# Kernel tuning notes

Measured on AMD Instinct MI355X. Metric: run time of the kernel, lower is better.

Reference implementation:

```python
import jax, jax.numpy as jnp
import numpy as np

SHIFTS = 1
WINDOW_SIZES = (4, 8, 16)
BN_EPS = 1e-5


def _calc_attn_path(x, ws, shifts):
    # x: (b, H, W, 2c) with channels laid out as (qv=2, c)
    b, H, W, c2 = x.shape
    c = c2 // 2
    if shifts > 0:
        x = jnp.roll(x, shift=(-ws // 2, -ws // 2), axis=(1, 2))
    h, w = H // ws, W // ws
    # 'b (h dh) (w dw) (qv c) -> qv (b h w) (dh dw c)'
    qv = x.reshape(b, h, ws, w, ws, 2, c).transpose(5, 0, 1, 3, 2, 4, 6)
    qv = qv.reshape(2, b * h * w, ws * ws * c)
    q, v = qv[0], qv[1]                       # (N, D), N = b*h*w windows, D = ws*ws*c
    atn = jax.nn.softmax(q @ q.T, axis=-1)    # (N, N) attention across windows (as in source)
    y = atn @ v                               # (N, D)
    # '(b h w) (dh dw c) -> b (h dh) (w dw) c'
    y = y.reshape(b, h, w, ws, ws, c).transpose(0, 1, 3, 2, 4, 5).reshape(b, H, W, c)
    if shifts > 0:
        y = jnp.roll(y, shift=(ws // 2, ws // 2), axis=(1, 2))
    return y, atn


def setup_inputs() -> dict:
    key = jax.random.key(0)
    ks = jax.random.split(key, 3)
    B, H, W, C = 4, 128, 128, 180
    inputs = jax.random.normal(ks[0], (B, H, W, C), jnp.float32)
    conv1_w = jax.random.normal(ks[1], (1, 1, C, 2 * C), jnp.float32) * 0.05
    conv1_b = jnp.zeros((2 * C,), jnp.float32)
    bn_scale = jnp.ones((2 * C,), jnp.float32)
    bn_bias = jnp.zeros((2 * C,), jnp.float32)
    conv2_w = jax.random.normal(ks[2], (1, 1, C, C), jnp.float32) * 0.05
    conv2_b = jnp.zeros((C,), jnp.float32)
    return {"inputs": inputs, "conv1_w": conv1_w, "conv1_b": conv1_b,
            "bn_scale": bn_scale, "bn_bias": bn_bias,
            "conv2_w": conv2_w, "conv2_b": conv2_b}


def reference(inputs, conv1_w, conv1_b, bn_scale, bn_bias, conv2_w, conv2_b):
    # 1x1 conv to 2*C channels (calc_attn=True)
    x = jnp.einsum('bhwc,cd->bhwd', inputs, conv1_w[0, 0]) + conv1_b
    # BatchNorm in training mode (batch statistics)
    mean = x.mean(axis=(0, 1, 2))
    var = x.var(axis=(0, 1, 2))
    x = (x - mean) * jax.lax.rsqrt(var + BN_EPS) * bn_scale + bn_bias
    xs = jnp.split(x, 3, axis=-1)             # three groups of 2*C/3 channels
    ys, attns = [], []
    for ws, xi in zip(WINDOW_SIZES, xs):
        y, a = _calc_attn_path(xi, ws, SHIFTS)
        ys.append(y)
        attns.append(a)
    y = jnp.concatenate(ys, axis=-1)          # back to C channels
    y = jnp.einsum('bhwc,cd->bhwd', y, conv2_w[0, 0]) + conv2_b
    return (y, *attns)
```

## Files before the change

kernel.cpp:

```cpp
#include <hip/hip_runtime.h>

typedef unsigned short u16;
typedef __bf16 bf16x8 __attribute__((ext_vector_type(8)));
typedef float f32x4 __attribute__((ext_vector_type(4)));
typedef u16 u16x4 __attribute__((ext_vector_type(4)));
typedef u16 u16x8 __attribute__((ext_vector_type(8)));

__device__ __forceinline__ u16 f2bf(float v) {
    unsigned u = __float_as_uint(v);
    unsigned r = (u + 0x7fffu + ((u >> 16) & 1u)) >> 16;
    return (u16)r;
}
__device__ __forceinline__ float bf2f(u16 u) { return __uint_as_float(((unsigned)u) << 16); }

__device__ __forceinline__ void async_cp16(const u16* g, u16* l) {
    __builtin_amdgcn_global_load_lds((const __attribute__((address_space(1))) unsigned int*)g,
                                     (__attribute__((address_space(3))) unsigned int*)l, 16, 0, 0);
}

__global__ __launch_bounds__(256) void gemm_f32(
    const u16* __restrict__ A, const u16* __restrict__ B,
    float* __restrict__ C, const float* __restrict__ bias,
    int K, int ldc, int n_store)
{
    __shared__ char smem[16384];
    u16* As = (u16*)smem;
    u16* Bs = (u16*)(smem + 8192);
    const int tid = threadIdx.x;
    const int lane = tid & 63;
    const int wave = tid >> 6;
    const int wm = wave >> 1, wn = wave & 1;
    const long m0 = (long)blockIdx.y * 128;
    const long n0 = (long)blockIdx.x * 128;

    f32x4 acc[4][4] = {};
    const int lrow = tid >> 2;
    const int lk = (tid & 3) << 3;
    const u16* Ag = A + (m0 + lrow) * (long)K + lk;
    const u16* Bg = B + (n0 + lrow) * (long)K + lk;
    u16* Asl = As + tid * 8;
    u16* Bsl = Bs + tid * 8;
    const long K64 = (long)64 * K;

    for (int k0 = 0; k0 < K; k0 += 32) {
        async_cp16(Ag + k0, Asl);
        async_cp16(Ag + k0 + K64, Asl + 2048);
        async_cp16(Bg + k0, Bsl);
        async_cp16(Bg + k0 + K64, Bsl + 2048);
        __syncthreads();
        bf16x8 af[4], bg[4];
        const int ro = (lane & 15) * 32 + ((lane >> 4) << 3);
#pragma unroll
        for (int i = 0; i < 4; i++) af[i] = *(const bf16x8*)(As + (wm * 64 + i * 16) * 32 + ro);
#pragma unroll
        for (int j = 0; j < 4; j++) bg[j] = *(const bf16x8*)(Bs + (wn * 64 + j * 16) * 32 + ro);
#pragma unroll
        for (int i = 0; i < 4; i++)
#pragma unroll
            for (int j = 0; j < 4; j++)
                acc[i][j] = __builtin_amdgcn_mfma_f32_16x16x32_bf16(af[i], bg[j], acc[i][j], 0, 0, 0);
        __syncthreads();
    }

    float bv[4];
#pragma unroll
    for (int j = 0; j < 4; j++) bv[j] = bias[n0 + wn * 64 + j * 16 + (lane & 15)];

    float* Cs = (float*)smem;
    for (int c = 0; c < 4; c++) {
        __syncthreads();
        if (wm == (c >> 1)) {
#pragma unroll
            for (int ii = 0; ii < 2; ii++) {
                const int i = (c & 1) * 2 + ii;
#pragma unroll
                for (int j = 0; j < 4; j++)
#pragma unroll
                    for (int r = 0; r < 4; r++) {
                        const int lr = ii * 16 + ((lane >> 4) << 2) + r;
                        Cs[lr * 128 + wn * 64 + j * 16 + (lane & 15)] = acc[i][j][r] + bv[j];
                    }
            }
        }
        __syncthreads();
        const int lr = tid >> 3;
        const int cg = (tid & 7) * 16;
        const long rowg = m0 + c * 32 + lr;
#pragma unroll
        for (int e = 0; e < 4; e++) {
            const int colg = cg + e * 4;
            if ((int)n0 + colg < n_store)
                *(f32x4*)(C + rowg * (long)ldc + n0 + colg) = *(const f32x4*)(Cs + lr * 128 + colg);
        }
    }
}

__global__ __launch_bounds__(256) void conv1_gemm(
    const float* __restrict__ A, const u16* __restrict__ B,
    u16* __restrict__ C, const float* __restrict__ bias)
{
    __shared__ char smem[16384];
    u16* As = (u16*)smem;
    u16* Bs = (u16*)(smem + 8192);
    const int tid = threadIdx.x;
    const int lane = tid & 63;
    const int wave = tid >> 6;
    const int wm = wave >> 1, wn = wave & 1;
    const long m0 = (long)blockIdx.y * 128;
    const long n0 = (long)blockIdx.x * 128;

    f32x4 acc[4][4] = {};
    const int lrow = tid >> 2;
    const int lk = (tid & 3) << 3;
    const float* Ar0 = A + (m0 + lrow) * 180L;
    const float* Ar1 = Ar0 + 64 * 180L;
    const u16* Bg = B + (n0 + lrow) * 192L + lk;
    u16* Asl = As + tid * 8;
    u16* Bsl = Bs + tid * 8;

#pragma unroll
    for (int k0 = 0; k0 < 192; k0 += 32) {
        const int gk = k0 + lk;
        u16x8 oa, ob;
        if (gk + 8 <= 180) {
            f32x4 a0 = *(const f32x4*)(Ar0 + gk), a1 = *(const f32x4*)(Ar0 + gk + 4);
            f32x4 b0 = *(const f32x4*)(Ar1 + gk), b1 = *(const f32x4*)(Ar1 + gk + 4);
#pragma unroll
            for (int c = 0; c < 4; c++) {
                oa[c] = f2bf(a0[c]); oa[4 + c] = f2bf(a1[c]);
                ob[c] = f2bf(b0[c]); ob[4 + c] = f2bf(b1[c]);
            }
        } else if (gk < 180) {
            f32x4 a0 = *(const f32x4*)(Ar0 + gk);
            f32x4 b0 = *(const f32x4*)(Ar1 + gk);
#pragma unroll
            for (int c = 0; c < 4; c++) {
                oa[c] = f2bf(a0[c]); oa[4 + c] = 0;
                ob[c] = f2bf(b0[c]); ob[4 + c] = 0;
            }
        } else {
#pragma unroll
            for (int c = 0; c < 8; c++) { oa[c] = 0; ob[c] = 0; }
        }
        *(u16x8*)Asl = oa;
        *(u16x8*)(Asl + 2048) = ob;
        async_cp16(Bg + k0, Bsl);
        async_cp16(Bg + k0 + 64 * 192, Bsl + 2048);
        __syncthreads();
        bf16x8 af[4], bg[4];
        const int ro = (lane & 15) * 32 + ((lane >> 4) << 3);
#pragma unroll
        for (int i = 0; i < 4; i++) af[i] = *(const bf16x8*)(As + (wm * 64 + i * 16) * 32 + ro);
#pragma unroll
        for (int j = 0; j < 4; j++) bg[j] = *(const bf16x8*)(Bs + (wn * 64 + j * 16) * 32 + ro);
#pragma unroll
        for (int i = 0; i < 4; i++)
#pragma unroll
            for (int j = 0; j < 4; j++)
                acc[i][j] = __builtin_amdgcn_mfma_f32_16x16x32_bf16(af[i], bg[j], acc[i][j], 0, 0, 0);
        __syncthreads();
    }

    float bv[4];
#pragma unroll
    for (int j = 0; j < 4; j++) bv[j] = bias[n0 + wn * 64 + j * 16 + (lane & 15)];

    u16* Cs = (u16*)smem;
    for (int c = 0; c < 2; c++) {
        __syncthreads();
        if (wm == c) {
#pragma unroll
            for (int i = 0; i < 4; i++)
#pragma unroll
                for (int j = 0; j < 4; j++)
#pragma unroll
                    for (int r = 0; r < 4; r++) {
                        const int lr = i * 16 + ((lane >> 4) << 2) + r;
                        Cs[lr * 128 + wn * 64 + j * 16 + (lane & 15)] = f2bf(acc[i][j][r] + bv[j]);
                    }
        }
        __syncthreads();
        const int lr = tid >> 2;
        const int cg = (tid & 3) * 32;
        const long rowg = m0 + c * 64 + lr;
#pragma unroll
        for (int e = 0; e < 4; e++) {
            const int colg = cg + e * 8;
            *(u16x8*)(C + rowg * 384L + n0 + colg) = *(const u16x8*)(Cs + lr * 128 + colg);
        }
    }
}

__global__ __launch_bounds__(256) void qq_all(
    const u16* __restrict__ q0, const u16* __restrict__ q1, const u16* __restrict__ q2,
    float* __restrict__ S0, float* __restrict__ pG1, float* __restrict__ pG2)
{
    __shared__ char smem[16384];
    u16* As = (u16*)smem;
    u16* Bs = (u16*)(smem + 8192);
    const int bid = blockIdx.x;
    int seg, local;
    if (bid < 528) { seg = 0; local = bid; }
    else if (bid < 816) { seg = 1; local = bid - 528; }
    else { seg = 2; local = bid - 816; }
    const int tX = seg == 0 ? 32 : (seg == 1 ? 8 : 2);
    const int TT = (tX * (tX + 1)) >> 1;
    const int K = seg == 0 ? 1024 : (seg == 1 ? 3840 : 15360);
    const int Ksplit = seg == 0 ? 1024 : (seg == 1 ? 480 : 256);
    const int N = seg == 0 ? 4096 : (seg == 1 ? 1024 : 256);
    const u16* A = seg == 0 ? q0 : (seg == 1 ? q1 : q2);
    float* outP = seg == 0 ? S0 : (seg == 1 ? pG1 : pG2);
    const int z = local / TT;
    int rem = local - z * TT;
    int by = 0, rowlen = tX;
    while (rem >= rowlen) { rem -= rowlen; by++; rowlen--; }
    const int bx = by + rem;

    const int tid = threadIdx.x;
    const int lane = tid & 63;
    const int wave = tid >> 6;
    const int wm = wave >> 1, wn = wave & 1;
    const long m0 = (long)by * 128;
    const long n0 = (long)bx * 128;
    const int kbeg = z * Ksplit;

    f32x4 acc[4][4] = {};
    const int lrow = tid >> 2;
    const int lk = (tid & 3) << 3;
    const u16* Ag = A + (m0 + lrow) * (long)K + lk;
    const u16* Bg = A + (n0 + lrow) * (long)K + lk;
    u16* Asl = As + tid * 8;
    u16* Bsl = Bs + tid * 8;
    const long K64 = (long)64 * K;

    for (int k0 = kbeg; k0 < kbeg + Ksplit; k0 += 32) {
        async_cp16(Ag + k0, Asl);
        async_cp16(Ag + k0 + K64, Asl + 2048);
        async_cp16(Bg + k0, Bsl);
        async_cp16(Bg + k0 + K64, Bsl + 2048);
        __syncthreads();
        bf16x8 af[4], bg[4];
        const int ro = (lane & 15) * 32 + ((lane >> 4) << 3);
#pragma unroll
        for (int i = 0; i < 4; i++) af[i] = *(const bf16x8*)(As + (wm * 64 + i * 16) * 32 + ro);
#pragma unroll
        for (int j = 0; j < 4; j++) bg[j] = *(const bf16x8*)(Bs + (wn * 64 + j * 16) * 32 + ro);
#pragma unroll
        for (int i = 0; i < 4; i++)
#pragma unroll
            for (int j = 0; j < 4; j++)
                acc[i][j] = __builtin_amdgcn_mfma_f32_16x16x32_bf16(af[i], bg[j], acc[i][j], 0, 0, 0);
        __syncthreads();
    }

    float* Pz = outP + (long)z * N * N;

    if (bx != by) {
        const int r0 = (int)n0 + wn * 64 + (lane & 15);
        const int c0 = (int)m0 + wm * 64 + ((lane >> 4) << 2);
#pragma unroll
        for (int j = 0; j < 4; j++) {
            float* rp = Pz + (long)(r0 + j * 16) * N + c0;
#pragma unroll
            for (int i = 0; i < 4; i++)
                *(f32x4*)(rp + i * 16) = acc[i][j];
        }
    }

    float* Cs = (float*)smem;
    for (int c = 0; c < 4; c++) {
        __syncthreads();
        if (wm == (c >> 1)) {
#pragma unroll
            for (int ii = 0; ii < 2; ii++) {
                const int i = (c & 1) * 2 + ii;
#pragma unroll
                for (int j = 0; j < 4; j++)
#pragma unroll
                    for (int r = 0; r < 4; r++) {
                        const int lr = ii * 16 + ((lane >> 4) << 2) + r;
                        Cs[lr * 128 + wn * 64 + j * 16 + (lane & 15)] = acc[i][j][r];
                    }
            }
        }
        __syncthreads();
        const int lr = tid >> 3;
        const int cg = (tid & 7) * 16;
        const long rowg = m0 + c * 32 + lr;
#pragma unroll
        for (int e = 0; e < 4; e++) {
            const int colg = cg + e * 4;
            *(f32x4*)(Pz + rowg * (long)N + n0 + colg) = *(const f32x4*)(Cs + lr * 128 + colg);
        }
    }
}

__global__ __launch_bounds__(256, 4) void pv_all(
    const u16* __restrict__ a0, const u16* __restrict__ a1, const u16* __restrict__ a2,
    const u16* __restrict__ vt0, const u16* __restrict__ vt1, const u16* __restrict__ vt2,
    u16* __restrict__ Ysp, float* __restrict__ pP0, float* __restrict__ pP1)
{
    __shared__ char smem[16384];
    u16* As = (u16*)smem;
    u16* Bs = (u16*)(smem + 8192);
    const int bid = blockIdx.x;
    int seg, local, z = 0;
    if (bid < 512) { seg = 0; z = bid >> 8; local = bid & 255; }
    else if (bid < 752) { seg = 1; local = bid - 512; }
    else { seg = 2; local = bid - 752; }
    const int tX = seg == 0 ? 8 : (seg == 1 ? 30 : 120);
    const int K = seg == 0 ? 4096 : (seg == 1 ? 1024 : 256);
    const int Ksplit = seg == 0 ? 2048 : K;
    const int D = seg == 0 ? 960 : (seg == 1 ? 3840 : 15360);
    const int l2ws = 2 + seg;
    const int l2wc = 5 - seg;
    const u16* A = seg == 0 ? a0 : (seg == 1 ? a1 : a2);
    const u16* B = seg == 0 ? vt0 : (seg == 1 ? vt1 : vt2);
    const int bx = local % tX;
    const int by = local / tX;

    const int tid = threadIdx.x;
    const int lane = tid & 63;
    const int wave = tid >> 6;
    const int wm = wave >> 1, wn = wave & 1;
    const long m0 = (long)by * 128;
    const long n0 = (long)bx * 128;
    const int kbeg = z * Ksplit;

    f32x4 acc[4][4] = {};
    const int lrow = tid >> 2;
    const int lk = (tid & 3) << 3;
    const u16* Ag = A + (m0 + lrow) * (long)K + lk;
    const u16* Bg = B + (n0 + lrow) * (long)K + lk;
    u16* Asl = As + tid * 8;
    u16* Bsl = Bs + tid * 8;
    const long K64 = (long)64 * K;

    for (int k0 = kbeg; k0 < kbeg + Ksplit; k0 += 32) {
        async_cp16(Ag + k0, Asl);
        async_cp16(Ag + k0 + K64, Asl + 2048);
        async_cp16(Bg + k0, Bsl);
        async_cp16(Bg + k0 + K64, Bsl + 2048);
        __syncthreads();
        bf16x8 af[4], bg[4];
        const int ro = (lane & 15) * 32 + ((lane >> 4) << 3);
#pragma unroll
        for (int i = 0; i < 4; i++) af[i] = *(const bf16x8*)(As + (wm * 64 + i * 16) * 32 + ro);
#pragma unroll
        for (int j = 0; j < 4; j++) bg[j] = *(const bf16x8*)(Bs + (wn * 64 + j * 16) * 32 + ro);
#pragma unroll
        for (int i = 0; i < 4; i++)
#pragma unroll
            for (int j = 0; j < 4; j++)
                acc[i][j] = __builtin_amdgcn_mfma_f32_16x16x32_bf16(af[i], bg[j], acc[i][j], 0, 0, 0);
        __syncthreads();
    }

    if (seg == 0) {
        float* Pz = (z == 0) ? pP0 : pP1;
        float* Cs = (float*)smem;
        for (int c = 0; c < 4; c++) {
            __syncthreads();
            if (wm == (c >> 1)) {
#pragma unroll
                for (int ii = 0; ii < 2; ii++) {
                    const int i = (c & 1) * 2 + ii;
#pragma unroll
                    for (int j = 0; j < 4; j++)
#pragma unroll
                        for (int r = 0; r < 4; r++) {
                            const int lr = ii * 16 + ((lane >> 4) << 2) + r;
                            Cs[lr * 128 + wn * 64 + j * 16 + (lane & 15)] = acc[i][j][r];
                        }
                }
            }
            __syncthreads();
            const int lr = tid >> 3;
            const int cg = (tid & 7) * 16;
            const long rowg = m0 + c * 32 + lr;
#pragma unroll
            for (int e = 0; e < 4; e++) {
                const int colg = cg + e * 4;
                *(f32x4*)(Pz + rowg * 1024L + n0 + colg) = *(const f32x4*)(Cs + lr * 128 + colg);
            }
        }
        return;
    }

    u16* Cs = (u16*)smem;
    const int wcm = (1 << l2wc) - 1;
    const int wsm = (1 << l2ws) - 1;
    const int sh = 1 << (l2ws - 1);
    for (int c = 0; c < 2; c++) {
        __syncthreads();
        if (wm == c) {
#pragma unroll
            for (int i = 0; i < 4; i++)
#pragma unroll
                for (int j = 0; j < 4; j++)
#pragma unroll
                    for (int r = 0; r < 4; r++) {
                        const int lr = i * 16 + ((lane >> 4) << 2) + r;
                        Cs[lr * 128 + wn * 64 + j * 16 + (lane & 15)] = f2bf(acc[i][j][r]);
                    }
        }
        __syncthreads();
        const int lr = tid >> 2;
        const int cgbase = (tid & 3) * 32;
        const int n = (int)m0 + c * 64 + lr;
        const int wi = n & wcm;
        const int hi = (n >> l2wc) & wcm;
        const int bb = n >> (2 * l2wc);
        const int rowb = (hi << l2ws) + sh;
        const int colb = (wi << l2ws) + sh;
        const long bbase = (long)bb * 128 * 128 * 192 + 60 * seg;
#pragma unroll
        for (int e = 0; e < 8; e++) {
            const int colg = cgbase + e * 4;
            const int d = (int)n0 + colg;
            if (d < D) {
                const int cc = d % 60;
                const int pp = d / 60;
                const int dh = pp >> l2ws;
                const int dw = pp & wsm;
                const int row = (rowb + dh) & 127;
                const int col = (colb + dw) & 127;
                *(u16x4*)(Ysp + bbase + ((long)row * 128 + col) * 192 + cc) =
                    *(const u16x4*)(Cs + lr * 128 + colg);
            }
        }
    }
}

__global__ __launch_bounds__(256) void reduce_scatter_g0(
    const float* __restrict__ pP0, const float* __restrict__ pP1, u16* __restrict__ Ysp)
{
    const int n = blockIdx.x;
    const int d = threadIdx.x * 4;
    if (d >= 960) return;
    const long i = (long)n * 1024 + d;
    f32x4 s = *(const f32x4*)(pP0 + i) + *(const f32x4*)(pP1 + i);
    const int cc = d % 60;
    const int pp = d / 60;
    const int dh = pp >> 2;
    const int dw = pp & 3;
    const int wi = n & 31;
    const int hi = (n >> 5) & 31;
    const int b = n >> 10;
    const int row = ((hi << 2) + dh + 2) & 127;
    const int col = ((wi << 2) + dw + 2) & 127;
    u16x4 o;
#pragma unroll
    for (int c = 0; c < 4; c++) o[c] = f2bf(s[c]);
    *(u16x4*)(Ysp + ((long)((b << 7) + row) * 128 + col) * 192 + cc) = o;
}

__global__ __launch_bounds__(256) void zero_pad(u16* __restrict__ Ysp)
{
    const long r = (long)blockIdx.x * 256 + threadIdx.x;
    u16* p = Ysp + r * 192 + 180;
    const u16x4 z = {0, 0, 0, 0};
    *(u16x4*)(p) = z;
    *(u16x4*)(p + 4) = z;
    *(u16x4*)(p + 8) = z;
}

__global__ __launch_bounds__(192) void prep_all(
    const float* __restrict__ W1, const float* __restrict__ W2,
    const float* __restrict__ b1, const float* __restrict__ b2,
    u16* __restrict__ W1t, u16* __restrict__ W2t,
    float* __restrict__ b1p, float* __restrict__ b2p, float* __restrict__ accum)
{
    const int bid = blockIdx.x;
    const int t = threadIdx.x;
    if (bid < 384) {
        W1t[bid * 192 + t] = (bid < 360 && t < 180) ? f2bf(W1[t * 360 + bid]) : (u16)0;
    } else if (bid < 640) {
        const int n = bid - 384;
        W2t[n * 192 + t] = (n < 180 && t < 180) ? f2bf(W2[t * 180 + n]) : (u16)0;
    } else {
#pragma unroll
        for (int j = 0; j < 4; j++) {
            const int i = t + 192 * j;
            if (i < 384) b1p[i] = (i < 360) ? b1[i] : 0.0f;
            else if (i < 640) { const int k = i - 384; b2p[k] = (k < 180) ? b2[k] : 0.0f; }
            if (i < 768) accum[i] = 0.0f;
        }
    }
}

__global__ __launch_bounds__(384) void bn_stats(const u16* __restrict__ x, float* __restrict__ accum)
{
    const int ch = threadIdx.x;
    const long base = (long)blockIdx.x * 256 * 384;
    float s = 0.0f, s2 = 0.0f;
    for (int r = 0; r < 256; r++) {
        const float v = bf2f(x[base + (long)r * 384 + ch]);
        s += v; s2 += v * v;
    }
    atomicAdd(&accum[ch], s);
    atomicAdd(&accum[384 + ch], s2);
}

__global__ __launch_bounds__(256) void gather_all(
    const u16* __restrict__ x, const float* __restrict__ accum,
    const float* __restrict__ bns, const float* __restrict__ bnb,
    u16* __restrict__ q0, u16* __restrict__ q1, u16* __restrict__ q2,
    u16* __restrict__ vt0, u16* __restrict__ vt1, u16* __restrict__ vt2)
{
    __shared__ u16 t[64][65];
    const int bid = blockIdx.x;
    int seg, local;
    if (bid < 1024) { seg = 0; local = bid; }
    else if (bid < 1984) { seg = 1; local = bid - 1024; }
    else { seg = 2; local = bid - 1984; }
    const int tX = seg == 0 ? 16 : (seg == 1 ? 60 : 240);
    const int N = seg == 0 ? 4096 : (seg == 1 ? 1024 : 256);
    const int D = seg == 0 ? 960 : (seg == 1 ? 3840 : 15360);
    const int Dp = seg == 0 ? 1024 : (seg == 1 ? 3840 : 15360);
    const int l2ws = 2 + seg;
    const int l2wc = 5 - seg;
    u16* q = seg == 0 ? q0 : (seg == 1 ? q1 : q2);
    u16* vt = seg == 0 ? vt0 : (seg == 1 ? vt1 : vt2);
    const int bx = local % tX;
    const int by = local / tX;

    const int d0 = bx * 64;
    const int n0 = by * 64;
    const int tc = threadIdx.x & 63;
    const int tr = threadIdx.x >> 6;

    const int d = d0 + tc;
    const int sh = 1 << (l2ws - 1);
    const int cc = d % 60;
    const int pp = d / 60;
    const int dh = pp >> l2ws;
    const int dw = pp & ((1 << l2ws) - 1);
    const int wcm = (1 << l2wc) - 1;
    const int ch = 120 * seg + cc;
    const float m_q = accum[ch] * (1.0f / 65536.0f);
    const float v_q = accum[384 + ch] * (1.0f / 65536.0f) - m_q * m_q;
    const float seq = bns[ch] * rsqrtf(v_q + 1e-5f);
    const float beq = bnb[ch] - m_q * seq;
    const float m_v = accum[ch + 60] * (1.0f / 65536.0f);
    const float v_v = accum[384 + ch + 60] * (1.0f / 65536.0f) - m_v * m_v;
    const float sev = bns[ch + 60] * rsqrtf(v_v + 1e-5f);
    const float bev = bnb[ch + 60] - m_v * sev;
    const bool valid = d < D;

#pragma unroll 4
    for (int i = 0; i < 16; i++) {
        const int n = n0 + i * 4 + tr;
        const int wi = n & wcm;
        const int hi = (n >> l2wc) & wcm;
        const int b = n >> (2 * l2wc);
        const int row = ((hi << l2ws) + dh + sh) & 127;
        const int col = ((wi << l2ws) + dw + sh) & 127;
        const long src = ((long)((b << 7) + row) * 128 + col) * 384 + ch;
        const float xq = bf2f(x[src]);
        const float xv = bf2f(x[src + 60]);
        q[(long)n * Dp + d] = valid ? f2bf(seq * xq + beq) : (u16)0;
        t[tc][i * 4 + tr] = f2bf(sev * xv + bev);
    }
    __syncthreads();
#pragma unroll 4
    for (int i = 0; i < 16; i++) {
        const int dd = i * 4 + tr;
        vt[(long)(d0 + dd) * N + n0 + tc] = t[dd][tc];
    }
}

template <int VPT>
__device__ __forceinline__ void softmax_body(
    const float* __restrict__ P, int nsplit, long MN, int rowi,
    float* __restrict__ S, u16* __restrict__ Sb)
{
    const int N = VPT * 256;
    const long base = (long)rowi * N;
    float v[VPT];
    float mx = -3.0e38f;
#pragma unroll
    for (int i = 0; i < VPT; i++) {
        const long idx = base + i * 256 + threadIdx.x;
        float val = P[idx];
        for (int z = 1; z < nsplit; z++) val += P[(long)z * MN + idx];
        v[i] = val; mx = fmaxf(mx, val);
    }
#pragma unroll
    for (int o = 32; o > 0; o >>= 1) mx = fmaxf(mx, __shfl_down(mx, o, 64));
    __shared__ float redm[4];
    if ((threadIdx.x & 63) == 0) redm[threadIdx.x >> 6] = mx;
    __syncthreads();
    mx = fmaxf(fmaxf(redm[0], redm[1]), fmaxf(redm[2], redm[3]));
    float s = 0.0f;
#pragma unroll
    for (int i = 0; i < VPT; i++) { v[i] = __expf(v[i] - mx); s += v[i]; }
#pragma unroll
    for (int o = 32; o > 0; o >>= 1) s += __shfl_down(s, o, 64);
    __shared__ float reds[4];
    if ((threadIdx.x & 63) == 0) reds[threadIdx.x >> 6] = s;
    __syncthreads();
    s = reds[0] + reds[1] + reds[2] + reds[3];
    const float inv = 1.0f / s;
#pragma unroll
    for (int i = 0; i < VPT; i++) {
        const float r = v[i] * inv;
        const long idx = base + i * 256 + threadIdx.x;
        S[idx] = r;
        Sb[idx] = f2bf(r);
    }
}

__global__ __launch_bounds__(256) void softmax_all(
    float* __restrict__ S0, const float* __restrict__ pG1, const float* __restrict__ pG2,
    float* __restrict__ out1, float* __restrict__ out2,
    u16* __restrict__ ab0, u16* __restrict__ ab1, u16* __restrict__ ab2)
{
    const int r = blockIdx.x;
    if (r < 4096)      softmax_body<16>(S0, 1, 16777216L, r, S0, ab0);
    else if (r < 5120) softmax_body<4>(pG1, 8, 1048576L, r - 4096, out1, ab1);
    else               softmax_body<1>(pG2, 60, 65536L, r - 5120, out2, ab2);
}

extern "C" void kernel_launch(void* const* d_in, const int* in_sizes, int n_in,
                              void* d_out, int out_size, void* d_ws, size_t ws_size,
                              hipStream_t stream)
{
    const float* in_x = (const float*)d_in[0];
    const float* w1  = (const float*)d_in[1];
    const float* b1  = (const float*)d_in[2];
    const float* bns = (const float*)d_in[3];
    const float* bnb = (const float*)d_in[4];
    const float* w2  = (const float*)d_in[5];
    const float* b2  = (const float*)d_in[6];
    float* out = (float*)d_out;

    char* w = (char*)d_ws;
    u16* atnb0 = (u16*)w;
    size_t off = 33554432;
    u16* x = (u16*)(w + off);
    float* pG1 = (float*)(w + off);
    float* pG2 = (float*)(w + off + 33554432);
    u16* Ysp = (u16*)(w + off);
    float* pP1 = (float*)(w + off + 25165824);
    off += 50331648;
    u16* W1t = (u16*)(w + off);  off += 147456;
    u16* W2t = (u16*)(w + off);  off += 98304;
    float* b1p = (float*)(w + off);   off += 4096;
    float* b2p = (float*)(w + off);   off += 4096;
    float* accum = (float*)(w + off); off += 4096;
    u16* q0 = (u16*)(w + off);  off += 8388608;
    u16* q1 = (u16*)(w + off);  off += 7864320;
    u16* q2 = (u16*)(w + off);  off += 7864320;
    u16* vt0 = (u16*)(w + off); off += 8388608;
    u16* vt1 = (u16*)(w + off); off += 7864320;
    u16* vt2 = (u16*)(w + off); off += 7864320;
    u16* atnb1 = (u16*)(w + off); off += 2097152;
    u16* atnb2 = (u16*)(w + off); off += 131072;
    float* pP0 = (float*)q0;

    float* S0 = out + 11796480L;
    float* S1 = out + 28573696L;
    float* S2 = out + 29622272L;

    prep_all<<<641, 192, 0, stream>>>(w1, w2, b1, b2, W1t, W2t, b1p, b2p, accum);
    conv1_gemm<<<dim3(3, 512), 256, 0, stream>>>(in_x, W1t, x, b1p);
    bn_stats<<<256, 384, 0, stream>>>(x, accum);
    gather_all<<<2944, 256, 0, stream>>>(x, accum, bns, bnb, q0, q1, q2, vt0, vt1, vt2);
    qq_all<<<996, 256, 0, stream>>>(q0, q1, q2, S0, pG1, pG2);
    softmax_all<<<5376, 256, 0, stream>>>(S0, pG1, pG2, S1, S2, atnb0, atnb1, atnb2);
    zero_pad<<<256, 256, 0, stream>>>(Ysp);
    pv_all<<<992, 256, 0, stream>>>(atnb0, atnb1, atnb2, vt0, vt1, vt2, Ysp, pP0, pP1);
    reduce_scatter_g0<<<4096, 256, 0, stream>>>(pP0, pP1, Ysp);
    gemm_f32<<<dim3(2, 512), 256, 0, stream>>>(Ysp, W2t, out, b2p, 192, 180, 180);
}
```

Baseline: 458.3 us.

## Double-buffer LDS tiles in GEMM kernels and swizzle blocks across XCDs

The gemm_f32, qq_all and pv_all kernels now use two LDS buffers per operand. The async global-to-LDS copy for the next K step is issued before the MFMAs on the current step, so memory latency is meant to overlap compute instead of stalling on a barrier each iteration. The qq_all and pv_all block indices are also remapped so that consecutive logical tiles land on the same XCD, to improve L2 reuse of shared operand rows. The cost is doubled LDS per block (32 KB), which may lower occupancy. The implicit wait at each barrier may also limit how much of the load actually overlaps.

```diff
diff --git a/kernel.cpp b/kernel.cpp
--- a/kernel.cpp
+++ b/kernel.cpp
@@ -18,10 +18,108 @@
                                      (__attribute__((address_space(3))) unsigned int*)l, 16, 0, 0);
 }
 
+__device__ __forceinline__ int xcd_swz(int local, int n) {
+    const int q = n >> 3, r = n & 7;
+    const int xcd = local & 7, j = local >> 3;
+    const int base = xcd < r ? xcd * (q + 1) : r * (q + 1) + (xcd - r) * q;
+    return base + j;
+}
+
 __global__ __launch_bounds__(256) void gemm_f32(
     const u16* __restrict__ A, const u16* __restrict__ B,
     float* __restrict__ C, const float* __restrict__ bias,
     int K, int ldc, int n_store)
+{
+    __shared__ char smem[32768];
+    u16* As = (u16*)smem;
+    u16* Bs = (u16*)(smem + 8192);
+    const int tid = threadIdx.x;
+    const int lane = tid & 63;
+    const int wave = tid >> 6;
+    const int wm = wave >> 1, wn = wave & 1;
+    const long m0 = (long)blockIdx.y * 128;
+    const long n0 = (long)blockIdx.x * 128;
+
+    f32x4 acc[4][4] = {};
+    const int lrow = tid >> 2;
+    const int lk = (tid & 3) << 3;
+    const u16* Ag = A + (m0 + lrow) * (long)K + lk;
+    const u16* Bg = B + (n0 + lrow) * (long)K + lk;
+    u16* Asl = As + tid * 8;
+    u16* Bsl = Bs + tid * 8;
+    const long K64 = (long)64 * K;
+    const int ro = (lane & 15) * 32 + ((lane >> 4) << 3);
+    const int nsteps = K >> 5;
+
+    async_cp16(Ag, Asl);
+    async_cp16(Ag + K64, Asl + 2048);
+    async_cp16(Bg, Bsl);
+    async_cp16(Bg + K64, Bsl + 2048);
+    __syncthreads();
+
+    int cur = 0;
+    for (int s = 0; s < nsteps; s++) {
+        if (s + 1 < nsteps) {
+            const int kn = (s + 1) << 5;
+            u16* An = Asl + ((cur ^ 1) << 13);
+            u16* Bn = Bsl + ((cur ^ 1) << 13);
+            async_cp16(Ag + kn, An);
+            async_cp16(Ag + kn + K64, An + 2048);
+            async_cp16(Bg + kn, Bn);
+            async_cp16(Bg + kn + K64, Bn + 2048);
+        }
+        bf16x8 af[4], bg[4];
+        const u16* Asc = As + (cur << 13);
+        const u16* Bsc = Bs + (cur << 13);
+#pragma unroll
+        for (int i = 0; i < 4; i++) af[i] = *(const bf16x8*)(Asc + (wm * 64 + i * 16) * 32 + ro);
+#pragma unroll
+        for (int j = 0; j < 4; j++) bg[j] = *(const bf16x8*)(Bsc + (wn * 64 + j * 16) * 32 + ro);
+#pragma unroll
+        for (int i = 0; i < 4; i++)
+#pragma unroll
+            for (int j = 0; j < 4; j++)
+                acc[i][j] = __builtin_amdgcn_mfma_f32_16x16x32_bf16(af[i], bg[j], acc[i][j], 0, 0, 0);
+        __syncthreads();
+        cur ^= 1;
+    }
+
+    float bv[4];
+#pragma unroll
+    for (int j = 0; j < 4; j++) bv[j] = bias[n0 + wn * 64 + j * 16 + (lane & 15)];
+
+    float* Cs = (float*)smem;
+    for (int c = 0; c < 4; c++) {
+        __syncthreads();
+        if (wm == (c >> 1)) {
+#pragma unroll
+            for (int ii = 0; ii < 2; ii++) {
+                const int i = (c & 1) * 2 + ii;
+#pragma unroll
+                for (int j = 0; j < 4; j++)
+#pragma unroll
+                    for (int r = 0; r < 4; r++) {
+                        const int lr = ii * 16 + ((lane >> 4) << 2) + r;
+                        Cs[lr * 128 + wn * 64 + j * 16 + (lane & 15)] = acc[i][j][r] + bv[j];
+                    }
+            }
+        }
+        __syncthreads();
+        const int lr = tid >> 3;
+        const int cg = (tid & 7) * 16;
+        const long rowg = m0 + c * 32 + lr;
+#pragma unroll
+        for (int e = 0; e < 4; e++) {
+            const int colg = cg + e * 4;
+            if ((int)n0 + colg < n_store)
+                *(f32x4*)(C + rowg * (long)ldc + n0 + colg) = *(const f32x4*)(Cs + lr * 128 + colg);
+        }
+    }
+}
+
+__global__ __launch_bounds__(256) void conv1_gemm(
+    const float* __restrict__ A, const u16* __restrict__ B,
+    u16* __restrict__ C, const float* __restrict__ bias)
 {
     __shared__ char smem[16384];
     u16* As = (u16*)smem;
@@ -36,82 +134,6 @@
     f32x4 acc[4][4] = {};
     const int lrow = tid >> 2;
     const int lk = (tid & 3) << 3;
-    const u16* Ag = A + (m0 + lrow) * (long)K + lk;
-    const u16* Bg = B + (n0 + lrow) * (long)K + lk;
-    u16* Asl = As + tid * 8;
-    u16* Bsl = Bs + tid * 8;
-    const long K64 = (long)64 * K;
-
-    for (int k0 = 0; k0 < K; k0 += 32) {
-        async_cp16(Ag + k0, Asl);
-        async_cp16(Ag + k0 + K64, Asl + 2048);
-        async_cp16(Bg + k0, Bsl);
-        async_cp16(Bg + k0 + K64, Bsl + 2048);
-        __syncthreads();
-        bf16x8 af[4], bg[4];
-        const int ro = (lane & 15) * 32 + ((lane >> 4) << 3);
-#pragma unroll
-        for (int i = 0; i < 4; i++) af[i] = *(const bf16x8*)(As + (wm * 64 + i * 16) * 32 + ro);
-#pragma unroll
-        for (int j = 0; j < 4; j++) bg[j] = *(const bf16x8*)(Bs + (wn * 64 + j * 16) * 32 + ro);
-#pragma unroll
-        for (int i = 0; i < 4; i++)
-#pragma unroll
-            for (int j = 0; j < 4; j++)
-                acc[i][j] = __builtin_amdgcn_mfma_f32_16x16x32_bf16(af[i], bg[j], acc[i][j], 0, 0, 0);
-        __syncthreads();
-    }
-
-    float bv[4];
-#pragma unroll
-    for (int j = 0; j < 4; j++) bv[j] = bias[n0 + wn * 64 + j * 16 + (lane & 15)];
-
-    float* Cs = (float*)smem;
-    for (int c = 0; c < 4; c++) {
-        __syncthreads();
-        if (wm == (c >> 1)) {
-#pragma unroll
-            for (int ii = 0; ii < 2; ii++) {
-                const int i = (c & 1) * 2 + ii;
-#pragma unroll
-                for (int j = 0; j < 4; j++)
-#pragma unroll
-                    for (int r = 0; r < 4; r++) {
-                        const int lr = ii * 16 + ((lane >> 4) << 2) + r;
-                        Cs[lr * 128 + wn * 64 + j * 16 + (lane & 15)] = acc[i][j][r] + bv[j];
-                    }
-            }
-        }
-        __syncthreads();
-        const int lr = tid >> 3;
-        const int cg = (tid & 7) * 16;
-        const long rowg = m0 + c * 32 + lr;
-#pragma unroll
-        for (int e = 0; e < 4; e++) {
-            const int colg = cg + e * 4;
-            if ((int)n0 + colg < n_store)
-                *(f32x4*)(C + rowg * (long)ldc + n0 + colg) = *(const f32x4*)(Cs + lr * 128 + colg);
-        }
-    }
-}
-
-__global__ __launch_bounds__(256) void conv1_gemm(
-    const float* __restrict__ A, const u16* __restrict__ B,
-    u16* __restrict__ C, const float* __restrict__ bias)
-{
-    __shared__ char smem[16384];
-    u16* As = (u16*)smem;
-    u16* Bs = (u16*)(smem + 8192);
-    const int tid = threadIdx.x;
-    const int lane = tid & 63;
-    const int wave = tid >> 6;
-    const int wm = wave >> 1, wn = wave & 1;
-    const long m0 = (long)blockIdx.y * 128;
-    const long n0 = (long)blockIdx.x * 128;
-
-    f32x4 acc[4][4] = {};
-    const int lrow = tid >> 2;
-    const int lk = (tid & 3) << 3;
     const float* Ar0 = A + (m0 + lrow) * 180L;
     const float* Ar1 = Ar0 + 64 * 180L;
     const u16* Bg = B + (n0 + lrow) * 192L + lk;
@@ -195,14 +217,14 @@
     const u16* __restrict__ q0, const u16* __restrict__ q1, const u16* __restrict__ q2,
     float* __restrict__ S0, float* __restrict__ pG1, float* __restrict__ pG2)
 {
-    __shared__ char smem[16384];
+    __shared__ char smem[32768];
     u16* As = (u16*)smem;
     u16* Bs = (u16*)(smem + 8192);
     const int bid = blockIdx.x;
     int seg, local;
-    if (bid < 528) { seg = 0; local = bid; }
-    else if (bid < 816) { seg = 1; local = bid - 528; }
-    else { seg = 2; local = bid - 816; }
+    if (bid < 528) { seg = 0; local = xcd_swz(bid, 528); }
+    else if (bid < 816) { seg = 1; local = xcd_swz(bid - 528, 288); }
+    else { seg = 2; local = xcd_swz(bid - 816, 180); }
     const int tX = seg == 0 ? 32 : (seg == 1 ? 8 : 2);
     const int TT = (tX * (tX + 1)) >> 1;
     const int K = seg == 0 ? 1024 : (seg == 1 ? 3840 : 15360);
@@ -232,25 +254,40 @@
     u16* Asl = As + tid * 8;
     u16* Bsl = Bs + tid * 8;
     const long K64 = (long)64 * K;
-
-    for (int k0 = kbeg; k0 < kbeg + Ksplit; k0 += 32) {
-        async_cp16(Ag + k0, Asl);
-        async_cp16(Ag + k0 + K64, Asl + 2048);
-        async_cp16(Bg + k0, Bsl);
-        async_cp16(Bg + k0 + K64, Bsl + 2048);
-        __syncthreads();
+    const int ro = (lane & 15) * 32 + ((lane >> 4) << 3);
+    const int nsteps = Ksplit >> 5;
+
+    async_cp16(Ag + kbeg, Asl);
+    async_cp16(Ag + kbeg + K64, Asl + 2048);
+    async_cp16(Bg + kbeg, Bsl);
+    async_cp16(Bg + kbeg + K64, Bsl + 2048);
+    __syncthreads();
+
+    int cur = 0;
+    for (int s = 0; s < nsteps; s++) {
+        if (s + 1 < nsteps) {
+            const int kn = kbeg + ((s + 1) << 5);
+            u16* An = Asl + ((cur ^ 1) << 13);
+            u16* Bn = Bsl + ((cur ^ 1) << 13);
+            async_cp16(Ag + kn, An);
+            async_cp16(Ag + kn + K64, An + 2048);
+            async_cp16(Bg + kn, Bn);
+            async_cp16(Bg + kn + K64, Bn + 2048);
+        }
         bf16x8 af[4], bg[4];
-        const int ro = (lane & 15) * 32 + ((lane >> 4) << 3);
-#pragma unroll
-        for (int i = 0; i < 4; i++) af[i] = *(const bf16x8*)(As + (wm * 64 + i * 16) * 32 + ro);
-#pragma unroll
-        for (int j = 0; j < 4; j++) bg[j] = *(const bf16x8*)(Bs + (wn * 64 + j * 16) * 32 + ro);
+        const u16* Asc = As + (cur << 13);
+        const u16* Bsc = Bs + (cur << 13);
+#pragma unroll
+        for (int i = 0; i < 4; i++) af[i] = *(const bf16x8*)(Asc + (wm * 64 + i * 16) * 32 + ro);
+#pragma unroll
+        for (int j = 0; j < 4; j++) bg[j] = *(const bf16x8*)(Bsc + (wn * 64 + j * 16) * 32 + ro);
 #pragma unroll
         for (int i = 0; i < 4; i++)
 #pragma unroll
             for (int j = 0; j < 4; j++)
                 acc[i][j] = __builtin_amdgcn_mfma_f32_16x16x32_bf16(af[i], bg[j], acc[i][j], 0, 0, 0);
         __syncthreads();
+        cur ^= 1;
     }
 
     float* Pz = outP + (long)z * N * N;
@@ -300,14 +337,14 @@
     const u16* __restrict__ vt0, const u16* __restrict__ vt1, const u16* __restrict__ vt2,
     u16* __restrict__ Ysp, float* __restrict__ pP0, float* __restrict__ pP1)
 {
-    __shared__ char smem[16384];
+    __shared__ char smem[32768];
     u16* As = (u16*)smem;
     u16* Bs = (u16*)(smem + 8192);
     const int bid = blockIdx.x;
     int seg, local, z = 0;
-    if (bid < 512) { seg = 0; z = bid >> 8; local = bid & 255; }
-    else if (bid < 752) { seg = 1; local = bid - 512; }
-    else { seg = 2; local = bid - 752; }
+    if (bid < 512) { seg = 0; const int l = xcd_swz(bid, 512); z = l >> 8; local = l & 255; }
+    else if (bid < 752) { seg = 1; local = xcd_swz(bid - 512, 240); }
+    else { seg = 2; local = xcd_swz(bid - 752, 240); }
     const int tX = seg == 0 ? 8 : (seg == 1 ? 30 : 120);
     const int K = seg == 0 ? 4096 : (seg == 1 ? 1024 : 256);
     const int Ksplit = seg == 0 ? 2048 : K;
@@ -335,25 +372,40 @@
     u16* Asl = As + tid * 8;
     u16* Bsl = Bs + tid * 8;
     const long K64 = (long)64 * K;
-
-    for (int k0 = kbeg; k0 < kbeg + Ksplit; k0 += 32) {
-        async_cp16(Ag + k0, Asl);
-        async_cp16(Ag + k0 + K64, Asl + 2048);
-        async_cp16(Bg + k0, Bsl);
-        async_cp16(Bg + k0 + K64, Bsl + 2048);
-        __syncthreads();
+    const int ro = (lane & 15) * 32 + ((lane >> 4) << 3);
+    const int nsteps = Ksplit >> 5;
+
+    async_cp16(Ag + kbeg, Asl);
+    async_cp16(Ag + kbeg + K64, Asl + 2048);
+    async_cp16(Bg + kbeg, Bsl);
+    async_cp16(Bg + kbeg + K64, Bsl + 2048);
+    __syncthreads();
+
+    int cur = 0;
+    for (int s = 0; s < nsteps; s++) {
+        if (s + 1 < nsteps) {
+            const int kn = kbeg + ((s + 1) << 5);
+            u16* An = Asl + ((cur ^ 1) << 13);
+            u16* Bn = Bsl + ((cur ^ 1) << 13);
+            async_cp16(Ag + kn, An);
+            async_cp16(Ag + kn + K64, An + 2048);
+            async_cp16(Bg + kn, Bn);
+            async_cp16(Bg + kn + K64, Bn + 2048);
+        }
         bf16x8 af[4], bg[4];
-        const int ro = (lane & 15) * 32 + ((lane >> 4) << 3);
-#pragma unroll
-        for (int i = 0; i < 4; i++) af[i] = *(const bf16x8*)(As + (wm * 64 + i * 16) * 32 + ro);
-#pragma unroll
-        for (int j = 0; j < 4; j++) bg[j] = *(const bf16x8*)(Bs + (wn * 64 + j * 16) * 32 + ro);
+        const u16* Asc = As + (cur << 13);
+        const u16* Bsc = Bs + (cur << 13);
+#pragma unroll
+        for (int i = 0; i < 4; i++) af[i] = *(const bf16x8*)(Asc + (wm * 64 + i * 16) * 32 + ro);
+#pragma unroll
+        for (int j = 0; j < 4; j++) bg[j] = *(const bf16x8*)(Bsc + (wn * 64 + j * 16) * 32 + ro);
 #pragma unroll
         for (int i = 0; i < 4; i++)
 #pragma unroll
             for (int j = 0; j < 4; j++)
                 acc[i][j] = __builtin_amdgcn_mfma_f32_16x16x32_bf16(af[i], bg[j], acc[i][j], 0, 0, 0);
         __syncthreads();
+        cur ^= 1;
     }
 
     if (seg == 0) {
```

After: 431.7 us. 5.8% less time.
